# Performance work log

Hardware: AMD Instinct MI355X
Metric: run time of the kernel (lower is better)

The kernel has to match this reference:

```python
import jax, jax.numpy as jnp
import numpy as np

B, S, HID = 1, 2048, 2048
NUM_HEADS, NUM_KV_HEADS, HEAD_DIM = 16, 4, 128
ROPE_THETA = 10000.0
EPS = 1e-6


def setup_inputs() -> dict:
    key = jax.random.key(0)
    ks = jax.random.split(key, 9)
    s = 0.02
    return {
        "hidden_states": jax.random.normal(ks[0], (B, S, HID), jnp.float32),
        "mu_prev": jax.random.normal(ks[1], (B, S, HID), jnp.float32),
        "wq": jax.random.normal(ks[2], (NUM_HEADS * HEAD_DIM, HID), jnp.float32) * s,
        "wk": jax.random.normal(ks[3], (NUM_KV_HEADS * HEAD_DIM, HID), jnp.float32) * s,
        "wv": jax.random.normal(ks[4], (NUM_KV_HEADS * HEAD_DIM, HID), jnp.float32) * s,
        "wo": jax.random.normal(ks[5], (HID, NUM_HEADS * HEAD_DIM), jnp.float32) * s,
        "wmq": jax.random.normal(ks[6], (NUM_HEADS * HEAD_DIM, HID), jnp.float32) * (s * 0.1),
        "wmk": jax.random.normal(ks[7], (NUM_KV_HEADS * HEAD_DIM, HID), jnp.float32) * (s * 0.1),
        "wmv": jax.random.normal(ks[8], (NUM_KV_HEADS * HEAD_DIM, HID), jnp.float32) * (s * 0.1),
        "q_norm_w": jnp.ones((HEAD_DIM,), jnp.float32),
        "k_norm_w": jnp.ones((HEAD_DIM,), jnp.float32),
    }


def _rmsnorm(x, w):
    var = jnp.mean(jnp.square(x), axis=-1, keepdims=True)
    return x * jax.lax.rsqrt(var + EPS) * w


def _rope_cos_sin(seq_len, dtype):
    inv_freq = 1.0 / (ROPE_THETA ** (jnp.arange(0, HEAD_DIM, 2, dtype=jnp.float32) / HEAD_DIM))
    freqs = jnp.arange(seq_len, dtype=jnp.float32)[:, None] * inv_freq[None, :]  # [S, D/2]
    emb = jnp.concatenate([freqs, freqs], axis=-1)  # [S, D]
    return jnp.cos(emb).astype(dtype), jnp.sin(emb).astype(dtype)


def _rotate_half(x):
    x1, x2 = jnp.split(x, 2, axis=-1)
    return jnp.concatenate([-x2, x1], axis=-1)


def reference(hidden_states, mu_prev, wq, wk, wv, wo, wmq, wmk, wmv, q_norm_w, k_norm_w):
    b, s, _ = hidden_states.shape
    # Fused mu-guided QKV projections (cat(x, mu) @ cat(W, Wm)^T == x@W^T + mu@Wm^T)
    q = hidden_states @ wq.T + mu_prev @ wmq.T  # [B,S,H*D]
    k = hidden_states @ wk.T + mu_prev @ wmk.T  # [B,S,KV*D]
    v = hidden_states @ wv.T + mu_prev @ wmv.T
    q = q.reshape(b, s, NUM_HEADS, HEAD_DIM).transpose(0, 2, 1, 3)      # [B,H,S,D]
    k = k.reshape(b, s, NUM_KV_HEADS, HEAD_DIM).transpose(0, 2, 1, 3)   # [B,KV,S,D]
    v = v.reshape(b, s, NUM_KV_HEADS, HEAD_DIM).transpose(0, 2, 1, 3)
    # per-head QK RMSNorm
    q = _rmsnorm(q, q_norm_w)
    k = _rmsnorm(k, k_norm_w)
    # RoPE
    cos, sin = _rope_cos_sin(s, q.dtype)
    q = q * cos + _rotate_half(q) * sin
    k = k * cos + _rotate_half(k) * sin
    # GQA attention without materializing repeated K/V: group query heads
    g = NUM_HEADS // NUM_KV_HEADS
    qg = q.reshape(b, NUM_KV_HEADS, g, s, HEAD_DIM)
    scale = 1.0 / jnp.sqrt(jnp.asarray(HEAD_DIM, q.dtype))
    scores = jnp.einsum('bkgqd,bkld->bkgql', qg, k) * scale  # [B,KV,G,S,S]
    causal = jnp.tril(jnp.ones((s, s), bool))
    scores = jnp.where(causal, scores, jnp.asarray(-jnp.inf, scores.dtype))
    probs = jax.nn.softmax(scores.astype(jnp.float32), axis=-1).astype(q.dtype)
    out = jnp.einsum('bkgql,bkld->bkgqd', probs, v)  # [B,KV,G,S,D]
    out = out.reshape(b, NUM_HEADS, s, HEAD_DIM).transpose(0, 2, 1, 3).reshape(b, s, NUM_HEADS * HEAD_DIM)
    return out @ wo.T
```

## Files before the change

kernel.cpp:

```cpp
#include <hip/hip_runtime.h>
#include <math.h>

#define SEQ 2048
#define HID_DIM 2048
#define NH 16
#define NKV 4
#define HD 128
#define QS 3072

typedef float  f4v  __attribute__((ext_vector_type(4)));
typedef __bf16 bf8v __attribute__((ext_vector_type(8)));
typedef __bf16 bf4v __attribute__((ext_vector_type(4)));
typedef __bf16 bf2v __attribute__((ext_vector_type(2)));

typedef __attribute__((address_space(1))) const void* gvp;
typedef __attribute__((address_space(3))) void*       svp;

__device__ __forceinline__ void gld16(const void* g, void* lds_wave_base) {
    __builtin_amdgcn_global_load_lds((gvp)g, (svp)lds_wave_base, 16, 0, 0);
}

__global__ __launch_bounds__(256)
void cvt_cat2(__bf16* __restrict__ dst, const float* __restrict__ s0,
              const float* __restrict__ s1, int rows, int kq)
{
    int i = blockIdx.x * 256 + threadIdx.x;
    if (i >= rows * kq * 2) return;
    int row = i / (2 * kq), c = i - row * 2 * kq;
    const float* s = (c < kq) ? s0 + ((size_t)row * kq + c) * 4
                              : s1 + ((size_t)row * kq + (c - kq)) * 4;
    float4 v = *reinterpret_cast<const float4*>(s);
    *reinterpret_cast<bf4v*>(dst + ((size_t)row * 2 * kq + c) * 4) =
        bf4v{ (__bf16)v.x, (__bf16)v.y, (__bf16)v.z, (__bf16)v.w };
}

__global__ __launch_bounds__(256)
void cvt(__bf16* __restrict__ dst, const float* __restrict__ src, int n4)
{
    int i = blockIdx.x * 256 + threadIdx.x;
    if (i >= n4) return;
    float4 v = *reinterpret_cast<const float4*>(src + (size_t)i * 4);
    *reinterpret_cast<bf4v*>(dst + (size_t)i * 4) =
        bf4v{ (__bf16)v.x, (__bf16)v.y, (__bf16)v.z, (__bf16)v.w };
}

__global__ __launch_bounds__(256)
void gemm_nt_sp(const __bf16* __restrict__ A, const __bf16* __restrict__ B,
                __bf16* __restrict__ P, int M, int N, int K, int KS)
{
    __shared__ __bf16 As[128 * 32];
    __shared__ __bf16 Bs[128 * 32];
    const int tid = threadIdx.x, lane = tid & 63, w = tid >> 6;
    const int wm = w >> 1, wn = w & 1;
    const int mm = lane & 15, quad = lane >> 4;
    const int m0 = blockIdx.y * 128, n0 = blockIdx.x * 128;
    const int kz0 = blockIdx.z * KS;
    const int r0 = lane >> 2, c0 = (lane & 3) * 8;

    f4v acc[4][4] = {};

    for (int k0 = kz0; k0 < kz0 + KS; k0 += 32) {
#pragma unroll
        for (int j = 0; j < 2; ++j) {
            int chunk = w * 2 + j;
            int row   = chunk * 16 + r0;
            gld16(&A[(size_t)(m0 + row) * K + k0 + c0], (char*)As + chunk * 1024);
            gld16(&B[(size_t)(n0 + row) * K + k0 + c0], (char*)Bs + chunk * 1024);
        }
        __syncthreads();
        bf8v af[4], bfv[4];
#pragma unroll
        for (int t = 0; t < 4; ++t) {
            af[t]  = *reinterpret_cast<const bf8v*>(&As[(wm * 64 + t * 16 + mm) * 32 + quad * 8]);
            bfv[t] = *reinterpret_cast<const bf8v*>(&Bs[(wn * 64 + t * 16 + mm) * 32 + quad * 8]);
        }
#pragma unroll
        for (int mt = 0; mt < 4; ++mt)
#pragma unroll
            for (int nt = 0; nt < 4; ++nt)
                acc[mt][nt] = __builtin_amdgcn_mfma_f32_16x16x32_bf16(af[mt], bfv[nt], acc[mt][nt], 0, 0, 0);
        __syncthreads();
    }
    __bf16* Pz = P + (size_t)blockIdx.z * M * N;
#pragma unroll
    for (int mt = 0; mt < 4; ++mt)
#pragma unroll
        for (int nt = 0; nt < 4; ++nt)
#pragma unroll
            for (int r = 0; r < 4; ++r)
                Pz[(size_t)(m0 + wm * 64 + mt * 16 + quad * 4 + r) * N
                   + n0 + wn * 64 + nt * 16 + mm] = (__bf16)acc[mt][nt][r];
}

__global__ __launch_bounds__(256)
void add4(const __bf16* __restrict__ P, float* __restrict__ out, int n4)
{
    int i = blockIdx.x * 256 + threadIdx.x;
    if (i >= n4) return;
    float4 s = {0.f, 0.f, 0.f, 0.f};
#pragma unroll
    for (int z = 0; z < 4; ++z) {
        bf4v v = *reinterpret_cast<const bf4v*>(P + (size_t)z * n4 * 4 + (size_t)i * 4);
        s.x += (float)v[0]; s.y += (float)v[1]; s.z += (float)v[2]; s.w += (float)v[3];
    }
    *reinterpret_cast<float4*>(out + (size_t)i * 4) = s;
}

__global__ __launch_bounds__(64)
void norm_rope(__bf16* __restrict__ qkv ,
               const __bf16* __restrict__ p1,
               const float* __restrict__ qw, const float* __restrict__ kw)
{
    const int s = blockIdx.x, hh = blockIdx.y, l = threadIdx.x;
    const float* wn; float scale; int off;
    if (hh < NH) { off = hh * HD;               wn = qw; scale = 0.08838834764831845f; }
    else         { off = 2048 + (hh - NH) * HD; wn = kw; scale = 1.0f; }
    __bf16* p = qkv + (size_t)s * QS + off;
    const __bf16* q1 = p1 + (size_t)s * QS + off;
    float x0 = (float)p[l]      + (float)q1[l];
    float x1 = (float)p[l + 64] + (float)q1[l + 64];
    float ss = x0 * x0 + x1 * x1;
#pragma unroll
    for (int o = 32; o; o >>= 1) ss += __shfl_xor(ss, o);
    float inv = rsqrtf(ss * (1.0f / 128.0f) + 1e-6f);
    x0 *= inv * wn[l];
    x1 *= inv * wn[l + 64];
    float invf = exp2f(-(float)l * (13.287712379549449f / 64.0f));
    float ang  = (float)s * invf;
    float c, sn;
    sincosf(ang, &sn, &c);
    p[l]      = (__bf16)((x0 * c - x1 * sn) * scale);
    p[l + 64] = (__bf16)((x1 * c + x0 * sn) * scale);
}

__global__ __launch_bounds__(256)
void pack_k(const __bf16* __restrict__ qkv, __bf16* __restrict__ Kt)
{
    const int kt = blockIdx.x, kh = blockIdx.y, t = threadIdx.x;
    char* tile = (char*)Kt + ((size_t)(kh * 32 + kt)) * 16384;
    const __bf16* src = qkv + 2048 + kh * HD;
#pragma unroll
    for (int i = 0; i < 4; ++i) {
        int cid = t * 4 + i;
        int key = cid >> 4, pc = cid & 15;
        int c = pc ^ (key & 15);
        bf8v v = *reinterpret_cast<const bf8v*>(src + (size_t)(kt * 64 + key) * QS + c * 8);
        *reinterpret_cast<bf8v*>(tile + cid * 16) = v;
    }
}

__global__ __launch_bounds__(256)
void pack_v(const __bf16* __restrict__ qkv0, const __bf16* __restrict__ qkv1,
            __bf16* __restrict__ Vt)
{
    const int kt = blockIdx.x, kh = blockIdx.y, t = threadIdx.x;
    char* tile = (char*)Vt + ((size_t)(kh * 32 + kt)) * 16384;
    const __bf16* s0 = qkv0 + 2560 + kh * HD;
    const __bf16* s1 = qkv1 + 2560 + kh * HD;
#pragma unroll
    for (int i = 0; i < 4; ++i) {
        int cid = t * 4 + i;
        int d = cid >> 3, kcp = cid & 7;
        int kc = kcp ^ (d & 7);
        size_t base = (size_t)(kt * 64 + kc * 8) * QS + d;
        __bf16 tmp[8];
#pragma unroll
        for (int j = 0; j < 8; ++j)
            tmp[j] = (__bf16)((float)s0[base + (size_t)j * QS] +
                              (float)s1[base + (size_t)j * QS]);
        *reinterpret_cast<bf8v*>(tile + cid * 16) = *reinterpret_cast<bf8v*>(tmp);
    }
}

__global__ __launch_bounds__(256)
void attn_split(const __bf16* __restrict__ qkv,
                const __bf16* __restrict__ Kt, const __bf16* __restrict__ Vt,
                __bf16* __restrict__ Op, float* __restrict__ Lp)
{
    __shared__ char Ks[16384];
    __shared__ char Vs[16384];
    __shared__ char Ps[4][2048];

    const int c = blockIdx.x, qt = 31 - blockIdx.y, h = blockIdx.z;
    if (c * 8 > qt) return;
    const int kend = min(qt, c * 8 + 7);
    const int tid = threadIdx.x, lane = tid & 63, w = tid >> 6;
    const int mm = lane & 15, quad = lane >> 4;
    const int kh = h >> 2;

    bf8v aq[4];
    const __bf16* qbase = qkv + (size_t)(qt * 64 + w * 16 + mm) * QS + h * HD;
#pragma unroll
    for (int ks = 0; ks < 4; ++ks)
        aq[ks] = *reinterpret_cast<const bf8v*>(qbase + ks * 32 + quad * 8);

    float lp[4] = {};
    f4v oacc[8] = {};

    for (int kt = c * 8; kt <= kend; ++kt) {
        __syncthreads();
        const char* ktile = (const char*)Kt + ((size_t)(kh * 32 + kt)) * 16384;
        const char* vtile = (const char*)Vt + ((size_t)(kh * 32 + kt)) * 16384;
#pragma unroll
        for (int j = 0; j < 4; ++j) {
            int chunk = w * 4 + j;
            gld16(ktile + chunk * 1024 + lane * 16, Ks + chunk * 1024);
            gld16(vtile + chunk * 1024 + lane * 16, Vs + chunk * 1024);
        }
        __syncthreads();

        f4v s[4] = {};
#pragma unroll
        for (int ks = 0; ks < 4; ++ks)
#pragma unroll
            for (int c16 = 0; c16 < 4; ++c16) {
                bf8v b = *reinterpret_cast<const bf8v*>(
                    Ks + (c16 * 16 + mm) * 256 + (((ks * 4 + quad) ^ mm) << 4));
                s[c16] = __builtin_amdgcn_mfma_f32_16x16x32_bf16(aq[ks], b, s[c16], 0, 0, 0);
            }
        if (kt == qt) {
#pragma unroll
            for (int c16 = 0; c16 < 4; ++c16)
#pragma unroll
                for (int r = 0; r < 4; ++r)
                    if (c16 * 16 + mm > w * 16 + quad * 4 + r)
                        s[c16][r] = -__builtin_inff();
        }
        float pr[4][4];
#pragma unroll
        for (int c16 = 0; c16 < 4; ++c16)
#pragma unroll
            for (int r = 0; r < 4; ++r) {
                pr[c16][r] = __expf(s[c16][r]);
                lp[r] += pr[c16][r];
            }
#pragma unroll
        for (int c16 = 0; c16 < 4; ++c16)
#pragma unroll
            for (int r = 0; r < 4; ++r) {
                float mine  = pr[c16][r];
                float other = __shfl_xor(mine, 1);
                if ((mm & 1) == 0) {
                    int roww = quad * 4 + r;
                    int cc   = c16 * 2 + (mm >> 3);
                    *reinterpret_cast<bf2v*>(
                        &Ps[w][roww * 128 + ((cc ^ (roww & 7)) << 4) + (mm & 7) * 2]) =
                        bf2v{ (__bf16)mine, (__bf16)other };
                }
            }
        bf8v pa[2];
#pragma unroll
        for (int kb = 0; kb < 2; ++kb)
            pa[kb] = *reinterpret_cast<const bf8v*>(
                &Ps[w][mm * 128 + (((kb * 4 + quad) ^ (mm & 7)) << 4)]);
#pragma unroll
        for (int nb = 0; nb < 8; ++nb) {
            int d = nb * 16 + mm;
#pragma unroll
            for (int kb = 0; kb < 2; ++kb) {
                bf8v bv = *reinterpret_cast<const bf8v*>(
                    Vs + d * 128 + (((kb * 4 + quad) ^ (d & 7)) << 4));
                oacc[nb] = __builtin_amdgcn_mfma_f32_16x16x32_bf16(pa[kb], bv, oacc[nb], 0, 0, 0);
            }
        }
    }
#pragma unroll
    for (int off = 1; off < 16; off <<= 1)
#pragma unroll
        for (int r = 0; r < 4; ++r) lp[r] += __shfl_xor(lp[r], off);
#pragma unroll
    for (int r = 0; r < 4; ++r) {
        int row = qt * 64 + w * 16 + quad * 4 + r;
        size_t obase = ((size_t)(c * 16 + h) * SEQ + row) * HD;
#pragma unroll
        for (int nb = 0; nb < 8; ++nb)
            Op[obase + nb * 16 + mm] = (__bf16)oacc[nb][r];
        if (mm == 0)
            Lp[(size_t)(c * 16 + h) * SEQ + row] = lp[r];
    }
}

__global__ __launch_bounds__(64)
void combine(const __bf16* __restrict__ Op, const float* __restrict__ Lp,
             __bf16* __restrict__ ab)
{
    const int row = blockIdx.x, h = blockIdx.y, l = threadIdx.x;
    const int nch = (row >> 9) + 1;
    float L = 0.f, a0 = 0.f, a1 = 0.f;
    for (int c = 0; c < nch; ++c) {
        L += Lp[(size_t)(c * 16 + h) * SEQ + row];
        bf2v p = *reinterpret_cast<const bf2v*>(
            Op + ((size_t)(c * 16 + h) * SEQ + row) * HD + 2 * l);
        a0 += (float)p[0];
        a1 += (float)p[1];
    }
    float inv = 1.f / L;
    *reinterpret_cast<bf2v*>(ab + (size_t)row * (NH * HD) + h * HD + 2 * l) =
        bf2v{ (__bf16)(a0 * inv), (__bf16)(a1 * inv) };
}

extern "C" void kernel_launch(void* const* d_in, const int* in_sizes, int n_in,
                              void* d_out, int out_size, void* d_ws, size_t ws_size,
                              hipStream_t stream)
{
    const float* hs  = (const float*)d_in[0];
    const float* mu  = (const float*)d_in[1];
    const float* wq  = (const float*)d_in[2];
    const float* wk  = (const float*)d_in[3];
    const float* wv  = (const float*)d_in[4];
    const float* wo  = (const float*)d_in[5];
    const float* wmq = (const float*)d_in[6];
    const float* wmk = (const float*)d_in[7];
    const float* wmv = (const float*)d_in[8];
    const float* qw  = (const float*)d_in[9];
    const float* kw  = (const float*)d_in[10];
    float* out = (float*)d_out;

    char* ws = (char*)d_ws;
    __bf16* Wcat = (__bf16*)(ws + 0);
    __bf16* Acat = (__bf16*)(ws + 25165824);
    __bf16* Wo   = (__bf16*)(ws + 41943040);
    __bf16* qkvp = (__bf16*)(ws + 50331648);
    __bf16* ab   = (__bf16*)(ws + 75497472);
    __bf16* Ktl  = (__bf16*)(ws + 0);
    __bf16* Vtl  = (__bf16*)(ws + 2097152);
    __bf16* Opart= (__bf16*)(ws + 4194304);
    float*  Lpart= (float*) (ws + 37748736);
    __bf16* outp = (__bf16*)(ws + 0);

    cvt_cat2<<<dim3((2048 * 1024 + 255) / 256), 256, 0, stream>>>(Acat, hs, mu, 2048, 512);
    cvt_cat2<<<dim3((2048 * 1024 + 255) / 256), 256, 0, stream>>>(Wcat, wq, wmq, 2048, 512);
    cvt_cat2<<<dim3((512 * 1024 + 255) / 256), 256, 0, stream>>>(Wcat + (size_t)2048 * 4096, wk, wmk, 512, 512);
    cvt_cat2<<<dim3((512 * 1024 + 255) / 256), 256, 0, stream>>>(Wcat + (size_t)2560 * 4096, wv, wmv, 512, 512);
    cvt<<<dim3((1024 * 1024 + 255) / 256), 256, 0, stream>>>(Wo, wo, 1024 * 1024);

    gemm_nt_sp<<<dim3(QS / 128, SEQ / 128, 2), 256, 0, stream>>>(Acat, Wcat, qkvp, SEQ, QS, 2 * HID_DIM, HID_DIM);
    norm_rope<<<dim3(SEQ, NH + NKV), dim3(64), 0, stream>>>(qkvp, qkvp + (size_t)SEQ * QS, qw, kw);
    pack_k<<<dim3(32, NKV), 256, 0, stream>>>(qkvp, Ktl);
    pack_v<<<dim3(32, NKV), 256, 0, stream>>>(qkvp, qkvp + (size_t)SEQ * QS, Vtl);
    attn_split<<<dim3(4, 32, NH), 256, 0, stream>>>(qkvp, Ktl, Vtl, Opart, Lpart);
    combine<<<dim3(SEQ, NH), 64, 0, stream>>>(Opart, Lpart, ab);
    gemm_nt_sp<<<dim3(HID_DIM / 128, SEQ / 128, 4), 256, 0, stream>>>(ab, Wo, outp, SEQ, HID_DIM, NH * HD, 512);
    add4<<<dim3((1024 * 1024 + 255) / 256), 256, 0, stream>>>(outp, out, 1024 * 1024);
}
```

Before: 366.3 us.

## Replace split-K GEMM with 256x256 double-buffered 8-wave pipelined MFMA kernel

Replaces the 128x128 single-buffered GEMM with a 256x256-tile, 512-thread kernel. It double-buffers 64-wide K tiles in 128KB of LDS, using XOR-swizzled layouts and manual vmcnt/lgkmcnt waits with raw barriers. Global-to-LDS loads are interleaved with MFMA quadrants, and setprio raises MFMA priority. The aim is to hide load latency and raise arithmetic intensity per block, but the grid gets much smaller (e.g. 12x8x2 blocks for QKV), so CU occupancy may suffer.

New measurement: 359.7 us. About the same (-1.8%).

```diff
diff --git a/kernel.cpp b/kernel.cpp
--- a/kernel.cpp
+++ b/kernel.cpp
@@ -19,6 +19,15 @@
 __device__ __forceinline__ void gld16(const void* g, void* lds_wave_base) {
     __builtin_amdgcn_global_load_lds((gvp)g, (svp)lds_wave_base, 16, 0, 0);
 }
+
+__device__ __forceinline__ void wgb() {
+    asm volatile("" ::: "memory");
+    __builtin_amdgcn_s_barrier();
+    asm volatile("" ::: "memory");
+}
+#define LGKM0 do { asm volatile("s_waitcnt lgkmcnt(0)" ::: "memory"); \
+                   __builtin_amdgcn_sched_barrier(0); } while (0)
+#define VMC(n) asm volatile("s_waitcnt vmcnt(" #n ")" ::: "memory")
 
 __global__ __launch_bounds__(256)
 void cvt_cat2(__bf16* __restrict__ dst, const float* __restrict__ s0,
@@ -44,51 +53,129 @@
         bf4v{ (__bf16)v.x, (__bf16)v.y, (__bf16)v.z, (__bf16)v.w };
 }
 
-__global__ __launch_bounds__(256)
-void gemm_nt_sp(const __bf16* __restrict__ A, const __bf16* __restrict__ B,
+__device__ __forceinline__ void stage_half(
+    const __bf16* __restrict__ g, int ldk, int row0, int ktile, int half,
+    char* buf, int w, int sr, int sc)
+{
+#pragma unroll
+    for (int j = 0; j < 2; ++j) {
+        int sid = w * 2 + j;
+        int rb = half * 8 + (sid >> 1), cb = sid & 1;
+        gld16(g + (size_t)(row0 + rb * 16 + sr) * ldk + ktile * 64 + cb * 32 + sc,
+              buf + (rb * 2 + cb) * 1024);
+    }
+}
+
+#define LOAD_A(BUF, MTB) \
+    _Pragma("unroll") for (int mt = 0; mt < 4; ++mt) \
+    _Pragma("unroll") for (int ks = 0; ks < 2; ++ks) \
+        a[mt][ks] = *(const bf8v*)((BUF) + (((wm * 8 + (MTB) + mt) * 2 + ks) << 10) + frag_off);
+#define LOAD_B(BUF, NTB, BR) \
+    _Pragma("unroll") for (int nt = 0; nt < 2; ++nt) \
+    _Pragma("unroll") for (int ks = 0; ks < 2; ++ks) \
+        BR[nt][ks] = *(const bf8v*)((BUF) + (((wn * 4 + (NTB) + nt) * 2 + ks) << 10) + frag_off);
+#define MFMA_Q(MTB, NTB, BR) \
+    __builtin_amdgcn_s_setprio(1); \
+    _Pragma("unroll") for (int mt = 0; mt < 4; ++mt) \
+    _Pragma("unroll") for (int nt = 0; nt < 2; ++nt) \
+    _Pragma("unroll") for (int ks = 0; ks < 2; ++ks) \
+        acc[(MTB) + mt][(NTB) + nt] = __builtin_amdgcn_mfma_f32_16x16x32_bf16( \
+            a[mt][ks], BR[nt][ks], acc[(MTB) + mt][(NTB) + nt], 0, 0, 0); \
+    __builtin_amdgcn_s_setprio(0);
+
+__global__ __launch_bounds__(512, 2)
+void gemm_nt_8p(const __bf16* __restrict__ A, const __bf16* __restrict__ B,
                 __bf16* __restrict__ P, int M, int N, int K, int KS)
 {
-    __shared__ __bf16 As[128 * 32];
-    __shared__ __bf16 Bs[128 * 32];
+    __shared__ __align__(1024) char lds[131072];
+    char* A0 = lds;
+    char* A1 = lds + 32768;
+    char* B0 = lds + 65536;
+    char* B1 = lds + 98304;
+
     const int tid = threadIdx.x, lane = tid & 63, w = tid >> 6;
-    const int wm = w >> 1, wn = w & 1;
+    const int wm = w >> 2, wn = w & 3;
     const int mm = lane & 15, quad = lane >> 4;
-    const int m0 = blockIdx.y * 128, n0 = blockIdx.x * 128;
-    const int kz0 = blockIdx.z * KS;
-    const int r0 = lane >> 2, c0 = (lane & 3) * 8;
-
-    f4v acc[4][4] = {};
-
-    for (int k0 = kz0; k0 < kz0 + KS; k0 += 32) {
-#pragma unroll
-        for (int j = 0; j < 2; ++j) {
-            int chunk = w * 2 + j;
-            int row   = chunk * 16 + r0;
-            gld16(&A[(size_t)(m0 + row) * K + k0 + c0], (char*)As + chunk * 1024);
-            gld16(&B[(size_t)(n0 + row) * K + k0 + c0], (char*)Bs + chunk * 1024);
+    const int m0 = blockIdx.y * 256, n0 = blockIdx.x * 256;
+    const int kt0 = (blockIdx.z * KS) >> 6;
+    const int T = KS >> 6;
+
+    const int g2 = lane ^ ((lane >> 4) & 3);
+    const int sr = g2 >> 2, sc = (g2 & 3) * 8;
+    const int gl = mm * 4 + quad;
+    const int frag_off = (gl ^ ((gl >> 4) & 3)) << 4;
+
+    f4v acc[8][4] = {};
+    bf8v a[4][2], b01[2][2], b23[2][2];
+
+    stage_half(A, K, m0, kt0,     0, A0, w, sr, sc);
+    stage_half(A, K, m0, kt0,     1, A0, w, sr, sc);
+    stage_half(B, K, n0, kt0,     0, B0, w, sr, sc);
+    stage_half(B, K, n0, kt0,     1, B0, w, sr, sc);
+    stage_half(A, K, m0, kt0 + 1, 0, A1, w, sr, sc);
+    stage_half(A, K, m0, kt0 + 1, 1, A1, w, sr, sc);
+    stage_half(B, K, n0, kt0 + 1, 0, B1, w, sr, sc);
+    stage_half(B, K, n0, kt0 + 1, 1, B1, w, sr, sc);
+    VMC(8);
+    wgb();
+
+    for (int t = 0; t < T; t += 2) {
+        const bool more = (t + 2) < T;
+        const int t2 = kt0 + t + 2, t3 = kt0 + t + 3;
+        LOAD_A(A0, 0)
+        LOAD_B(B0, 0, b01)
+        wgb(); LGKM0;
+        MFMA_Q(0, 0, b01)
+        wgb();
+        LOAD_B(B0, 2, b23)
+        wgb(); LGKM0;
+        MFMA_Q(0, 2, b23)
+        wgb();
+        LOAD_A(A0, 4)
+        if (more) stage_half(B, K, n0, t2, 0, B0, w, sr, sc);
+        wgb(); LGKM0;
+        MFMA_Q(4, 2, b23)
+        wgb();
+        if (more) {
+            stage_half(B, K, n0, t2, 1, B0, w, sr, sc);
+            stage_half(A, K, m0, t2, 0, A0, w, sr, sc);
         }
-        __syncthreads();
-        bf8v af[4], bfv[4];
-#pragma unroll
-        for (int t = 0; t < 4; ++t) {
-            af[t]  = *reinterpret_cast<const bf8v*>(&As[(wm * 64 + t * 16 + mm) * 32 + quad * 8]);
-            bfv[t] = *reinterpret_cast<const bf8v*>(&Bs[(wn * 64 + t * 16 + mm) * 32 + quad * 8]);
+        MFMA_Q(4, 0, b01)
+        if (more) { VMC(6); } else { VMC(0); }
+        wgb();
+        LOAD_A(A1, 0)
+        LOAD_B(B1, 0, b01)
+        if (more) stage_half(A, K, m0, t2, 1, A0, w, sr, sc);
+        wgb(); LGKM0;
+        MFMA_Q(0, 0, b01)
+        wgb();
+        LOAD_B(B1, 2, b23)
+        wgb(); LGKM0;
+        MFMA_Q(0, 2, b23)
+        wgb();
+        LOAD_A(A1, 4)
+        if (more) stage_half(B, K, n0, t3, 0, B1, w, sr, sc);
+        wgb(); LGKM0;
+        MFMA_Q(4, 2, b23)
+        wgb();
+        if (more) {
+            stage_half(B, K, n0, t3, 1, B1, w, sr, sc);
+            stage_half(A, K, m0, t3, 0, A1, w, sr, sc);
+            stage_half(A, K, m0, t3, 1, A1, w, sr, sc);
         }
-#pragma unroll
-        for (int mt = 0; mt < 4; ++mt)
-#pragma unroll
-            for (int nt = 0; nt < 4; ++nt)
-                acc[mt][nt] = __builtin_amdgcn_mfma_f32_16x16x32_bf16(af[mt], bfv[nt], acc[mt][nt], 0, 0, 0);
-        __syncthreads();
-    }
+        MFMA_Q(4, 0, b01)
+        if (more) { VMC(8); }
+        wgb();
+    }
+
     __bf16* Pz = P + (size_t)blockIdx.z * M * N;
 #pragma unroll
-    for (int mt = 0; mt < 4; ++mt)
+    for (int mt = 0; mt < 8; ++mt)
 #pragma unroll
         for (int nt = 0; nt < 4; ++nt)
 #pragma unroll
             for (int r = 0; r < 4; ++r)
-                Pz[(size_t)(m0 + wm * 64 + mt * 16 + quad * 4 + r) * N
+                Pz[(size_t)(m0 + wm * 128 + mt * 16 + quad * 4 + r) * N
                    + n0 + wn * 64 + nt * 16 + mm] = (__bf16)acc[mt][nt][r];
 }
 
@@ -334,12 +421,12 @@
     cvt_cat2<<<dim3((512 * 1024 + 255) / 256), 256, 0, stream>>>(Wcat + (size_t)2560 * 4096, wv, wmv, 512, 512);
     cvt<<<dim3((1024 * 1024 + 255) / 256), 256, 0, stream>>>(Wo, wo, 1024 * 1024);
 
-    gemm_nt_sp<<<dim3(QS / 128, SEQ / 128, 2), 256, 0, stream>>>(Acat, Wcat, qkvp, SEQ, QS, 2 * HID_DIM, HID_DIM);
+    gemm_nt_8p<<<dim3(QS / 256, SEQ / 256, 2), 512, 0, stream>>>(Acat, Wcat, qkvp, SEQ, QS, 2 * HID_DIM, HID_DIM);
     norm_rope<<<dim3(SEQ, NH + NKV), dim3(64), 0, stream>>>(qkvp, qkvp + (size_t)SEQ * QS, qw, kw);
     pack_k<<<dim3(32, NKV), 256, 0, stream>>>(qkvp, Ktl);
     pack_v<<<dim3(32, NKV), 256, 0, stream>>>(qkvp, qkvp + (size_t)SEQ * QS, Vtl);
     attn_split<<<dim3(4, 32, NH), 256, 0, stream>>>(qkvp, Ktl, Vtl, Opart, Lpart);
     combine<<<dim3(SEQ, NH), 64, 0, stream>>>(Opart, Lpart, ab);
-    gemm_nt_sp<<<dim3(HID_DIM / 128, SEQ / 128, 4), 256, 0, stream>>>(ab, Wo, outp, SEQ, HID_DIM, NH * HD, 512);
+    gemm_nt_8p<<<dim3(HID_DIM / 256, SEQ / 256, 4), 512, 0, stream>>>(ab, Wo, outp, SEQ, HID_DIM, NH * HD, 512);
     add4<<<dim3((1024 * 1024 + 255) / 256), 256, 0, stream>>>(outp, out, 1024 * 1024);
 }
```
